# Kernel tuning notes

Measured on AMD Instinct MI355X. Metric: run time of the kernel, lower is better.

Reference implementation:

```python
import jax, jax.numpy as jnp
import numpy as np

EPS = 1e-3  # keras BatchNormalization default epsilon


def _ngf(atoms, bonds, edges, W, b):
    """NeuralGraphHidden: neighbor gather + per-degree dense.
    atoms [B,N,Fa], bonds [B,N,D,Fb], edges [B,N,D] (-1 padded),
    W [D+1, Fa+Fb, width], b [D+1, width] -> [B,N,width]."""
    B, N, Fa = atoms.shape
    D = edges.shape[-1]
    deg = jnp.sum(edges != -1, axis=-1)  # [B,N] atom degrees
    # zero-row padded lookup table so edge index -1 gathers zeros
    apad = jnp.concatenate([jnp.zeros((B, 1, Fa), atoms.dtype), atoms], axis=1)
    neigh = jax.vmap(lambda a, e: a[e])(apad, edges + 1)  # [B,N,D,Fa]
    summed_atom = atoms + neigh.sum(axis=2)  # include_self=True
    summed_bond = bonds.sum(axis=2)
    feats = jnp.concatenate([summed_atom, summed_bond], axis=-1)  # [B,N,Fa+Fb]
    # dense transform for every degree, then select by actual degree
    all_out = jnp.einsum('bnf,dfw->bdnw', feats, W) + b[None, :, None, :]
    mask = (deg[:, None, :] == jnp.arange(D + 1)[None, :, None]).astype(atoms.dtype)
    return jnp.einsum('bdnw,bdn->bnw', all_out, mask)


def _bn(x, g, beta, m, v):
    return g * (x - m) * jax.lax.rsqrt(v + EPS) + beta


def setup_inputs() -> dict:
    key = jax.random.key(0)
    ks = jax.random.split(key, 32)
    B, N, D, Fa, Fb = 1024, 60, 5, 62, 6
    widths = [128, 128, 128]
    KSZ, FILT = 16, 128

    atoms = jax.random.normal(ks[0], (B, N, Fa), jnp.float32)
    bonds = jax.random.uniform(ks[1], (B, N, D, Fb), dtype=jnp.float32)
    edges = jax.random.randint(ks[2], (B, N, D), -1, N).astype(jnp.int32)

    def glorot(k, shape):
        s = jnp.sqrt(2.0 / (shape[-2] + shape[-1])).astype(jnp.float32)
        return jax.random.normal(k, shape, jnp.float32) * s

    inp = dict(atoms=atoms, bonds=bonds, edges=edges)
    fins = [Fa + Fb, widths[0] + Fb, widths[1] + Fb]
    for i in range(3):
        inp['W%d' % (i + 1)] = glorot(ks[3 + i], (D + 1, fins[i], widths[i]))
        inp['b%d' % (i + 1)] = 0.01 * jax.random.normal(ks[6 + i], (D + 1, widths[i]), jnp.float32)
    inp['Wc'] = glorot(ks[9], (KSZ, widths[2], FILT))
    for i, c in enumerate([widths[0], widths[1], widths[2], FILT]):
        inp['bn%d_g' % (i + 1)] = 1.0 + 0.1 * jax.random.normal(ks[10 + i], (c,), jnp.float32)
        inp['bn%d_b' % (i + 1)] = 0.1 * jax.random.normal(ks[14 + i], (c,), jnp.float32)
        inp['bn%d_m' % (i + 1)] = 0.1 * jax.random.normal(ks[18 + i], (c,), jnp.float32)
        inp['bn%d_v' % (i + 1)] = jax.random.uniform(ks[22 + i], (c,), jnp.float32, 0.5, 1.5)
    return inp


def reference(atoms, bonds, edges, W1, b1, W2, b2, W3, b3, Wc,
              bn1_g, bn1_b, bn1_m, bn1_v, bn2_g, bn2_b, bn2_m, bn2_v,
              bn3_g, bn3_b, bn3_m, bn3_v, bn4_g, bn4_b, bn4_m, bn4_v):
    x = jax.nn.relu(_bn(_ngf(atoms, bonds, edges, W1, b1), bn1_g, bn1_b, bn1_m, bn1_v))
    x = jax.nn.relu(_bn(_ngf(x, bonds, edges, W2, b2), bn2_g, bn2_b, bn2_m, bn2_v))
    x = jax.nn.relu(_bn(_ngf(x, bonds, edges, W3, b3), bn3_g, bn3_b, bn3_m, bn3_v))
    # Conv1D over the atom axis, VALID padding, no bias
    x = jax.lax.conv_general_dilated(x, Wc, window_strides=(1,), padding='VALID',
                                     dimension_numbers=('NWC', 'WIO', 'NWC'))
    x = jax.nn.relu(_bn(x, bn4_g, bn4_b, bn4_m, bn4_v))
    # dropout is identity at inference
    return x
```

## Files before the change

kernel.cpp:

```cpp
#include <hip/hip_runtime.h>
#include <hip/hip_bf16.h>

typedef __attribute__((ext_vector_type(8))) short bf16x8;
typedef __attribute__((ext_vector_type(4))) short short4v;
typedef __attribute__((ext_vector_type(4))) float f32x4;
typedef unsigned short u16;
typedef unsigned char u8;

static constexpr size_t OFF_BN   = 0;
static constexpr size_t OFF_SH2  = 4096;
static constexpr size_t OFF_BSUM = 13312;
static constexpr size_t OFF_WT1  = 750592;
static constexpr size_t OFF_WT2  = 898048;
static constexpr size_t OFF_WT3  = 1143808;
static constexpr size_t OFF_WCF  = 1389568;

__device__ __forceinline__ float bf2f(u16 r) {
  union { unsigned u; float f; } cv; cv.u = ((unsigned)r) << 16; return cv.f;
}
__device__ __forceinline__ u16 f2bf(float x) {
  __hip_bfloat16 h = __float2bfloat16(x); return *(u16*)&h;
}
__device__ __forceinline__ int fidx(int n, int c) {
  int u = c >> 3;
  int uu = (u < 16) ? (u ^ (n & 7)) : u;
  return n * 160 + (uu << 3) + (c & 7);
}

__device__ __forceinline__ void emit_wt(u16* dst, const float* W, int FIN, int FIN_A,
                                        int CB, int KSTEPS, int v) {
  int lane = v & 63;
  int ftile = (v >> 6) & 7;
  int ks = (v >> 9) % KSTEPS;
  int d = (v >> 9) / KSTEPS;
  int f = ftile * 16 + (lane & 15);
  int k0 = ks * 32 + (lane >> 4) * 8;
  bf16x8 o;
  #pragma unroll
  for (int i = 0; i < 8; ++i) {
    int k = k0 + i;
    int src = (k < FIN_A) ? k : (k >= CB && k < CB + 6) ? (FIN_A + k - CB) : -1;
    float x = (src >= 0) ? W[((size_t)d * FIN + src) * 128 + f] : 0.f;
    o[i] = (short)f2bf(x);
  }
  *reinterpret_cast<bf16x8*>(&dst[(size_t)v * 8]) = o;
}

__global__ __launch_bounds__(256) void prep(
    const float* __restrict__ bonds, const float* __restrict__ Wc,
    const float* __restrict__ W1, const float* __restrict__ W2, const float* __restrict__ W3,
    const float* g1, const float* be1, const float* m1, const float* v1,
    const float* g2, const float* be2, const float* m2, const float* v2,
    const float* g3, const float* be3, const float* m3, const float* v3,
    const float* g4, const float* be4, const float* m4, const float* v4,
    const float* bb1, const float* bb2, const float* bb3,
    float* __restrict__ scale, float* __restrict__ shift, float* __restrict__ shift2,
    u16* __restrict__ bsum, u16* __restrict__ wt1, u16* __restrict__ wt2,
    u16* __restrict__ wt3, u16* __restrict__ wcf) {
  __shared__ float sb[3840];
  const int b = blockIdx.x, tid = threadIdx.x;
  if (b < 480) {
    const int base = b * 128;
    const float4* src = (const float4*)(bonds + (size_t)base * 30);
    for (int i = tid; i < 960; i += 256) ((float4*)sb)[i] = src[i];
    __syncthreads();
    if (tid < 128) {
      float s[6] = {0.f, 0.f, 0.f, 0.f, 0.f, 0.f};
      #pragma unroll
      for (int d = 0; d < 5; ++d)
        #pragma unroll
        for (int j = 0; j < 6; ++j) s[j] += sb[tid * 30 + d * 6 + j];
      #pragma unroll
      for (int j = 0; j < 6; ++j) bsum[(size_t)(base + tid) * 6 + j] = f2bf(s[j]);
    }
  } else if (b < 608) {
    int v = (b - 480) * 256 + tid;
    int lane = v & 63, ftile = (v >> 6) & 7, ks = v >> 9;
    int f = ftile * 16 + (lane & 15);
    int k0 = ks * 32 + (lane >> 4) * 8;
    int tap = k0 >> 7, ch0 = k0 & 127;
    bf16x8 o;
    #pragma unroll
    for (int i = 0; i < 8; ++i)
      o[i] = (short)f2bf(Wc[((size_t)tap * 128 + ch0 + i) * 128 + f]);
    *reinterpret_cast<bf16x8*>(&wcf[(size_t)v * 8]) = o;
  } else if (b < 644) {
    emit_wt(wt1, W1, 68, 62, 64, 3, (b - 608) * 256 + tid);
  } else if (b < 704) {
    emit_wt(wt2, W2, 134, 128, 128, 5, (b - 644) * 256 + tid);
  } else if (b < 764) {
    emit_wt(wt3, W3, 134, 128, 128, 5, (b - 704) * 256 + tid);
  } else if (b < 766) {
    int idx = (b - 764) * 256 + tid;
    const float* gs[4] = {g1, g2, g3, g4};
    const float* bs[4] = {be1, be2, be3, be4};
    const float* ms[4] = {m1, m2, m3, m4};
    const float* vs[4] = {v1, v2, v3, v4};
    int l = idx >> 7, ch = idx & 127;
    float sc = gs[l][ch] / sqrtf(vs[l][ch] + 1e-3f);
    scale[idx] = sc;
    shift[idx] = bs[l][ch] - ms[l][ch] * sc;
  } else {
    int i = (b - 766) * 256 + tid;
    if (i < 2304) {
      const float* G[3] = {g1, g2, g3};
      const float* Be[3] = {be1, be2, be3};
      const float* M[3] = {m1, m2, m3};
      const float* V[3] = {v1, v2, v3};
      const float* Bl[3] = {bb1, bb2, bb3};
      int ll = i / 768, r = i % 768, f = r & 127;
      float sc = G[ll][f] / sqrtf(V[ll][f] + 1e-3f);
      float sh = Be[ll][f] - M[ll][f] * sc;
      shift2[i] = Bl[ll][r] * sc + sh;
    }
  }
}

template <int MPW, int CB, int KSTEPS, bool TOCONV>
__device__ __forceinline__ void layer(
    u16* __restrict__ feats, u16* __restrict__ xbt,
    const u8* __restrict__ S8, const u8* __restrict__ degs8,
    const int* __restrict__ presentS, const u16* __restrict__ bsum_b,
    const u16* __restrict__ wtf, const float* __restrict__ sc_l,
    const float* __restrict__ sh2_l, int tid, int lane, int wid) {
  const int fr = lane & 15, rg = lane >> 4;

  bf16x8 sf[4][2];
  #pragma unroll
  for (int nt = 0; nt < 4; ++nt) {
    #pragma unroll
    for (int ks = 0; ks < 2; ++ks) {
      int n = nt * 16 + fr, m0 = ks * 32 + rg * 8;
      const unsigned* wp = (const unsigned*)(S8 + n * 64 + m0);
      unsigned lo = wp[0], hi = wp[1];
      bf16x8 v;
      #pragma unroll
      for (int i = 0; i < 4; ++i) v[i] = (short)f2bf((float)((lo >> (i * 8)) & 255u));
      #pragma unroll
      for (int i = 0; i < 4; ++i) v[4 + i] = (short)f2bf((float)((hi >> (i * 8)) & 255u));
      sf[nt][ks] = v;
    }
  }

  f32x4 gacc[MPW][4];
  #pragma unroll
  for (int mt = 0; mt < MPW; ++mt)
    #pragma unroll
    for (int nt = 0; nt < 4; ++nt) gacc[mt][nt] = (f32x4){0.f, 0.f, 0.f, 0.f};
  #pragma unroll
  for (int mt = 0; mt < MPW; ++mt) {
    const int c = (wid * MPW + mt) * 16 + fr;
    #pragma unroll
    for (int ks = 0; ks < 2; ++ks) {
      const int m0 = ks * 32 + rg * 8;
      bf16x8 a = *reinterpret_cast<const bf16x8*>(
          &xbt[c * 64 + (((m0 >> 3) ^ (c & 7)) << 3)]);
      #pragma unroll
      for (int nt = 0; nt < 4; ++nt)
        gacc[mt][nt] = __builtin_amdgcn_mfma_f32_16x16x32_bf16(a, sf[nt][ks],
                                                               gacc[mt][nt], 0, 0, 0);
    }
  }
  #pragma unroll
  for (int mt = 0; mt < MPW; ++mt) {
    const int c0 = (wid * MPW + mt) * 16 + rg * 4;
    const int uu = c0 >> 3;
    #pragma unroll
    for (int nt = 0; nt < 4; ++nt) {
      const int n = nt * 16 + fr;
      if (n < 60) {
        short4v p;
        #pragma unroll
        for (int j = 0; j < 4; ++j) p[j] = (short)f2bf(gacc[mt][nt][j]);
        *reinterpret_cast<short4v*>(
            &feats[n * 160 + ((uu ^ (n & 7)) << 3) + (c0 & 7)]) = p;
      }
    }
  }
  for (int i = tid; i < 360; i += 256) {
    int n = i / 6, c = CB + (i % 6);
    feats[fidx(n, c)] = bsum_b[i];
  }
  __syncthreads();

  const int pres = *presentS;

  if constexpr (!TOCONV) {
    const int f0w = wid * 32;
    unsigned dgw[4];
    #pragma unroll
    for (int m = 0; m < 4; ++m)
      dgw[m] = *(const unsigned*)(degs8 + m * 16 + rg * 4);
    float scf[2] = {sc_l[f0w + fr], sc_l[f0w + 16 + fr]};
    f32x4 racc[4][2];
    #pragma unroll
    for (int m = 0; m < 4; ++m)
      #pragma unroll
      for (int nf = 0; nf < 2; ++nf) racc[m][nf] = (f32x4){0.f, 0.f, 0.f, 0.f};

    for (int d = 0; d < 6; ++d) {
      if (!(pres & (1 << d))) continue;
      const u16* __restrict__ wd = wtf + (size_t)d * (KSTEPS * 4096);
      f32x4 acc[4][2];
      #pragma unroll
      for (int m = 0; m < 4; ++m)
        #pragma unroll
        for (int nf = 0; nf < 2; ++nf) acc[m][nf] = (f32x4){0.f, 0.f, 0.f, 0.f};
      bf16x8 wring[2][2];
      #pragma unroll
      for (int nf = 0; nf < 2; ++nf)
        wring[0][nf] = *reinterpret_cast<const bf16x8*>(
            &wd[((0 * 8 + wid * 2 + nf) * 64 + lane) * 8]);
      #pragma unroll
      for (int nf = 0; nf < 2; ++nf)
        wring[1][nf] = *reinterpret_cast<const bf16x8*>(
            &wd[((1 * 8 + wid * 2 + nf) * 64 + lane) * 8]);
      #pragma unroll
      for (int ks = 0; ks < KSTEPS; ++ks) {
        bf16x8 afr[4];
        const int u = ks * 4 + rg;
        #pragma unroll
        for (int m = 0; m < 4; ++m) {
          const int n = m * 16 + fr;
          const int uu = (u < 16) ? (u ^ (n & 7)) : u;
          afr[m] = *reinterpret_cast<const bf16x8*>(&feats[n * 160 + (uu << 3)]);
        }
        #pragma unroll
        for (int m = 0; m < 4; ++m)
          #pragma unroll
          for (int nf = 0; nf < 2; ++nf)
            acc[m][nf] = __builtin_amdgcn_mfma_f32_16x16x32_bf16(
                afr[m], wring[ks & 1][nf], acc[m][nf], 0, 0, 0);
        if (ks + 2 < KSTEPS) {
          #pragma unroll
          for (int nf = 0; nf < 2; ++nf)
            wring[ks & 1][nf] = *reinterpret_cast<const bf16x8*>(
                &wd[(((ks + 2) * 8 + wid * 2 + nf) * 64 + lane) * 8]);
        }
      }
      #pragma unroll
      for (int nf = 0; nf < 2; ++nf) {
        const float sh = sh2_l[d * 128 + f0w + nf * 16 + fr];
        #pragma unroll
        for (int m = 0; m < 4; ++m) {
          #pragma unroll
          for (int j = 0; j < 4; ++j) {
            float y = fmaxf(acc[m][nf][j] * scf[nf] + sh, 0.f);
            bool sel = (((dgw[m] >> (8 * j)) & 255u) == (unsigned)d);
            racc[m][nf][j] = sel ? y : racc[m][nf][j];
          }
        }
      }
    }
    #pragma unroll
    for (int m = 0; m < 4; ++m) {
      const int n0 = m * 16 + rg * 4;
      if (n0 < 60) {
        #pragma unroll
        for (int nf = 0; nf < 2; ++nf) {
          const int c = f0w + nf * 16 + fr;
          short4v p;
          #pragma unroll
          for (int j = 0; j < 4; ++j) p[j] = (short)f2bf(racc[m][nf][j]);
          *reinterpret_cast<short4v*>(
              &xbt[c * 64 + (((n0 >> 3) ^ (c & 7)) << 3) + (n0 & 7)]) = p;
        }
      }
    }
  } else {
    int dgn[4];
    #pragma unroll
    for (int nt = 0; nt < 4; ++nt) dgn[nt] = degs8[nt * 16 + fr];
    f32x4 scv[2];
    #pragma unroll
    for (int mt = 0; mt < 2; ++mt)
      scv[mt] = *reinterpret_cast<const f32x4*>(&sc_l[(wid * 2 + mt) * 16 + rg * 4]);
    f32x4 racc[2][4];
    #pragma unroll
    for (int mt = 0; mt < 2; ++mt)
      #pragma unroll
      for (int nt = 0; nt < 4; ++nt) racc[mt][nt] = (f32x4){0.f, 0.f, 0.f, 0.f};

    for (int d = 0; d < 6; ++d) {
      if (!(pres & (1 << d))) continue;
      const u16* __restrict__ wd = wtf + (size_t)d * (KSTEPS * 4096);
      f32x4 acc[2][4];
      #pragma unroll
      for (int mt = 0; mt < 2; ++mt)
        #pragma unroll
        for (int nt = 0; nt < 4; ++nt) acc[mt][nt] = (f32x4){0.f, 0.f, 0.f, 0.f};
      bf16x8 wring[2][2];
      #pragma unroll
      for (int mt = 0; mt < 2; ++mt)
        wring[0][mt] = *reinterpret_cast<const bf16x8*>(
            &wd[((0 * 8 + wid * 2 + mt) * 64 + lane) * 8]);
      #pragma unroll
      for (int mt = 0; mt < 2; ++mt)
        wring[1][mt] = *reinterpret_cast<const bf16x8*>(
            &wd[((1 * 8 + wid * 2 + mt) * 64 + lane) * 8]);
      #pragma unroll
      for (int ks = 0; ks < KSTEPS; ++ks) {
        bf16x8 bfr[4];
        const int u = ks * 4 + rg;
        #pragma unroll
        for (int nt = 0; nt < 4; ++nt) {
          const int n = nt * 16 + fr;
          const int uu = (u < 16) ? (u ^ (n & 7)) : u;
          bfr[nt] = *reinterpret_cast<const bf16x8*>(&feats[n * 160 + (uu << 3)]);
        }
        #pragma unroll
        for (int mt = 0; mt < 2; ++mt)
          #pragma unroll
          for (int nt = 0; nt < 4; ++nt)
            acc[mt][nt] = __builtin_amdgcn_mfma_f32_16x16x32_bf16(
                wring[ks & 1][mt], bfr[nt], acc[mt][nt], 0, 0, 0);
        if (ks + 2 < KSTEPS) {
          #pragma unroll
          for (int mt = 0; mt < 2; ++mt)
            wring[ks & 1][mt] = *reinterpret_cast<const bf16x8*>(
                &wd[(((ks + 2) * 8 + wid * 2 + mt) * 64 + lane) * 8]);
        }
      }
      #pragma unroll
      for (int mt = 0; mt < 2; ++mt) {
        f32x4 shv = *reinterpret_cast<const f32x4*>(
            &sh2_l[d * 128 + (wid * 2 + mt) * 16 + rg * 4]);
        #pragma unroll
        for (int nt = 0; nt < 4; ++nt) {
          bool sel = (dgn[nt] == d);
          #pragma unroll
          for (int j = 0; j < 4; ++j) {
            float y = fmaxf(acc[mt][nt][j] * scv[mt][j] + shv[j], 0.f);
            racc[mt][nt][j] = sel ? y : racc[mt][nt][j];
          }
        }
      }
    }
    #pragma unroll
    for (int nt = 0; nt < 4; ++nt) {
      const int n = nt * 16 + fr;
      if (n < 60) {
        #pragma unroll
        for (int mt = 0; mt < 2; ++mt) {
          const int f0 = (wid * 2 + mt) * 16 + rg * 4;
          short4v p;
          #pragma unroll
          for (int j = 0; j < 4; ++j) p[j] = (short)f2bf(racc[mt][nt][j]);
          *reinterpret_cast<short4v*>(
              &xbt[n * 128 + (((f0 >> 3) ^ (n & 7)) << 3) + (f0 & 7)]) = p;
        }
      }
    }
  }
  __syncthreads();
}

__global__ __launch_bounds__(256, 4) void mega(
    const float* __restrict__ atoms, const int* __restrict__ edges_g,
    const u16* __restrict__ bsum, const u16* __restrict__ wt1,
    const u16* __restrict__ wt2, const u16* __restrict__ wt3,
    const u16* __restrict__ wcf, const float* __restrict__ scale,
    const float* __restrict__ shift, const float* __restrict__ shift2,
    float* __restrict__ out) {
  __shared__ __align__(16) char smem[39936];
  u16* feats = (u16*)smem;
  u16* xbt = (u16*)(smem + 19200);
  u8* S8 = (u8*)(smem + 35584);
  signed char* eds = (signed char*)(smem + 39424);
  u8* degs8 = (u8*)(smem + 39728);
  int* presentS = (int*)(smem + 39792);
  float* fscr = (float*)smem;

  const int b = blockIdx.x, tid = threadIdx.x;
  const int lane = tid & 63;
  const int wid = __builtin_amdgcn_readfirstlane(tid >> 6);

  if (tid == 0) *presentS = 0;
  for (int i = tid; i < 300; i += 256) eds[i] = (signed char)edges_g[b * 300 + i];
  {
    const float4* ag4 = (const float4*)(atoms + (size_t)b * 3720);
    float4* fs4 = (float4*)fscr;
    for (int i = tid; i < 930; i += 256) fs4[i] = ag4[i];
    int4 z4 = {0, 0, 0, 0};
    int4* xz = (int4*)(xbt + 64 * 64);
    for (int i = tid; i < 512; i += 256) xz[i] = z4;
    int4* sz = (int4*)S8;
    for (int i = tid; i < 240; i += 256) sz[i] = z4;
  }
  __syncthreads();

  if (tid < 64) {
    int dgv = 7;
    if (tid < 60) {
      dgv = 0;
      #pragma unroll
      for (int d = 0; d < 5; ++d) dgv += (eds[tid * 5 + d] >= 0);
      atomicOr(presentS, 1 << dgv);
      S8[tid * 64 + tid] = (u8)(S8[tid * 64 + tid] + 1);
      #pragma unroll
      for (int d = 0; d < 5; ++d) {
        int e = eds[tid * 5 + d];
        if (e >= 0) S8[tid * 64 + e] = (u8)(S8[tid * 64 + e] + 1);
      }
    }
    degs8[tid] = (u8)dgv;
  }
  for (int id = tid; id < 512; id += 256) {
    int oct = id & 7, c = id >> 3;
    bf16x8 v;
    #pragma unroll
    for (int k = 0; k < 8; ++k) {
      int n = oct * 8 + k;
      float x = (c < 62 && n < 60) ? fscr[n * 62 + c] : 0.f;
      v[k] = (short)f2bf(x);
    }
    *reinterpret_cast<bf16x8*>(&xbt[c * 64 + ((oct ^ (c & 7)) << 3)]) = v;
  }
  __syncthreads();

  for (int i = tid; i < 60 * 52; i += 256) {
    int n = i / 52, q = i % 52;
    int c = (q < 26) ? (70 + q) : (108 + q);
    feats[fidx(n, c)] = 0;
  }

  const u16* bsum_b = bsum + (size_t)b * 360;
  layer<1, 64, 3, false>(feats, xbt, S8, degs8, presentS, bsum_b, wt1,
                         scale + 0, shift2 + 0, tid, lane, wid);
  layer<2, 128, 5, false>(feats, xbt, S8, degs8, presentS, bsum_b, wt2,
                          scale + 128, shift2 + 768, tid, lane, wid);
  layer<2, 128, 5, true>(feats, xbt, S8, degs8, presentS, bsum_b, wt3,
                         scale + 256, shift2 + 1536, tid, lane, wid);

  {
    const int fr = lane & 15, rg = lane >> 4;
    const u16* xconv = xbt;
    f32x4 cacc[3][2];
    #pragma unroll
    for (int rt = 0; rt < 3; ++rt)
      #pragma unroll
      for (int ct = 0; ct < 2; ++ct) cacc[rt][ct] = (f32x4){0.f, 0.f, 0.f, 0.f};

    bf16x8 br[4][2], ar[2][3];
    auto loadB = [&](int ks, int slot) {
      #pragma unroll
      for (int nt = 0; nt < 2; ++nt)
        br[slot][nt] = *reinterpret_cast<const bf16x8*>(
            &wcf[(((size_t)ks * 8 + wid * 2 + nt) * 64 + lane) * 8]);
    };
    auto loadA = [&](int ks, int slot) {
      int rowadd = ks >> 2;
      int unit = ((ks & 3) << 2) + rg;
      #pragma unroll
      for (int rt = 0; rt < 3; ++rt) {
        int arow = rt * 16 + fr + rowadd;
        int uo = unit ^ (arow & 7);
        ar[slot][rt] = *reinterpret_cast<const bf16x8*>(&xconv[arow * 128 + uo * 8]);
      }
    };
    loadB(0, 0); loadB(1, 1); loadB(2, 2); loadA(0, 0);
    #pragma unroll 4
    for (int ks = 0; ks < 64; ++ks) {
      if (ks < 63) loadA(ks + 1, (ks + 1) & 1);
      #pragma unroll
      for (int rt = 0; rt < 3; ++rt)
        #pragma unroll
        for (int ct = 0; ct < 2; ++ct)
          cacc[rt][ct] = __builtin_amdgcn_mfma_f32_16x16x32_bf16(
              ar[ks & 1][rt], br[ks & 3][ct], cacc[rt][ct], 0, 0, 0);
      if (ks < 61) loadB(ks + 3, (ks + 3) & 3);
    }

    #pragma unroll
    for (int ct = 0; ct < 2; ++ct) {
      int f = wid * 32 + ct * 16 + fr;
      float sc = scale[384 + f], sh = shift[384 + f];
      #pragma unroll
      for (int rt = 0; rt < 3; ++rt) {
        #pragma unroll
        for (int j = 0; j < 4; ++j) {
          int t = rt * 16 + rg * 4 + j;
          if (t < 45) {
            float y = fmaxf(cacc[rt][ct][j] * sc + sh, 0.f);
            out[((size_t)b * 45 + t) * 128 + f] = y;
          }
        }
      }
    }
  }
}

extern "C" void kernel_launch(void* const* d_in, const int* in_sizes, int n_in,
                              void* d_out, int out_size, void* d_ws, size_t ws_size,
                              hipStream_t stream) {
  const float* atoms = (const float*)d_in[0];
  const float* bonds = (const float*)d_in[1];
  const int*   edges = (const int*)d_in[2];
  const float* W1 = (const float*)d_in[3]; const float* b1 = (const float*)d_in[4];
  const float* W2 = (const float*)d_in[5]; const float* b2 = (const float*)d_in[6];
  const float* W3 = (const float*)d_in[7]; const float* b3 = (const float*)d_in[8];
  const float* Wc = (const float*)d_in[9];

  char* ws = (char*)d_ws;
  float* scale  = (float*)(ws + OFF_BN);
  float* shift  = scale + 512;
  float* shift2 = (float*)(ws + OFF_SH2);
  u16*   bsum   = (u16*)(ws + OFF_BSUM);
  u16*   wt1    = (u16*)(ws + OFF_WT1);
  u16*   wt2    = (u16*)(ws + OFF_WT2);
  u16*   wt3    = (u16*)(ws + OFF_WT3);
  u16*   wcf    = (u16*)(ws + OFF_WCF);

  prep<<<775, 256, 0, stream>>>(
      bonds, Wc, W1, W2, W3,
      (const float*)d_in[10], (const float*)d_in[11], (const float*)d_in[12], (const float*)d_in[13],
      (const float*)d_in[14], (const float*)d_in[15], (const float*)d_in[16], (const float*)d_in[17],
      (const float*)d_in[18], (const float*)d_in[19], (const float*)d_in[20], (const float*)d_in[21],
      (const float*)d_in[22], (const float*)d_in[23], (const float*)d_in[24], (const float*)d_in[25],
      b1, b2, b3, scale, shift, shift2, bsum, wt1, wt2, wt3, wcf);

  mega<<<1024, 256, 0, stream>>>(atoms, edges, bsum, wt1, wt2, wt3, wcf,
                                 scale, shift, shift2, (float*)d_out);
}
```

Baseline: 202.9 us.

## Process two molecules per block and skip MFMA tiles without matching degree

Each block now handles two molecules with 512 threads, so each wave loads one weight fragment and reuses it across both molecules' atom tiles. A per-degree, per-16-row tile mask is built in shared memory, and MFMAs plus epilogue work are skipped for tiles with no atom of that degree. This cuts weight fetch traffic and redundant matrix work per molecule. In exchange it doubles LDS use per block (about 80KB), which lowers occupancy, and it adds divergent-free but branchy tile checks plus a union of degree-present masks across the two molecules.

```diff
diff --git a/kernel.cpp b/kernel.cpp
--- a/kernel.cpp
+++ b/kernel.cpp
@@ -120,10 +120,15 @@
 __device__ __forceinline__ void layer(
     u16* __restrict__ feats, u16* __restrict__ xbt,
     const u8* __restrict__ S8, const u8* __restrict__ degs8,
-    const int* __restrict__ presentS, const u16* __restrict__ bsum_b,
-    const u16* __restrict__ wtf, const float* __restrict__ sc_l,
-    const float* __restrict__ sh2_l, int tid, int lane, int wid) {
+    const int* __restrict__ presentS, const int* __restrict__ tilemask,
+    const u16* __restrict__ bsum2, const u16* __restrict__ wtf,
+    const float* __restrict__ sc_l, const float* __restrict__ sh2_l,
+    int tid, int lane, int w) {
   const int fr = lane & 15, rg = lane >> 4;
+  const int gmol = w & 1;
+  const u16* __restrict__ xm = xbt + gmol * 8192;
+  u16* __restrict__ fm = feats + gmol * 9600;
+  const u8* __restrict__ Sm = S8 + gmol * 4096;
 
   bf16x8 sf[4][2];
   #pragma unroll
@@ -131,7 +136,7 @@
     #pragma unroll
     for (int ks = 0; ks < 2; ++ks) {
       int n = nt * 16 + fr, m0 = ks * 32 + rg * 8;
-      const unsigned* wp = (const unsigned*)(S8 + n * 64 + m0);
+      const unsigned* wp = (const unsigned*)(Sm + n * 64 + m0);
       unsigned lo = wp[0], hi = wp[1];
       bf16x8 v;
       #pragma unroll
@@ -149,12 +154,12 @@
     for (int nt = 0; nt < 4; ++nt) gacc[mt][nt] = (f32x4){0.f, 0.f, 0.f, 0.f};
   #pragma unroll
   for (int mt = 0; mt < MPW; ++mt) {
-    const int c = (wid * MPW + mt) * 16 + fr;
+    const int c = ((w >> 1) * MPW + mt) * 16 + fr;
     #pragma unroll
     for (int ks = 0; ks < 2; ++ks) {
       const int m0 = ks * 32 + rg * 8;
       bf16x8 a = *reinterpret_cast<const bf16x8*>(
-          &xbt[c * 64 + (((m0 >> 3) ^ (c & 7)) << 3)]);
+          &xm[c * 64 + (((m0 >> 3) ^ (c & 7)) << 3)]);
       #pragma unroll
       for (int nt = 0; nt < 4; ++nt)
         gacc[mt][nt] = __builtin_amdgcn_mfma_f32_16x16x32_bf16(a, sf[nt][ks],
@@ -163,7 +168,7 @@
   }
   #pragma unroll
   for (int mt = 0; mt < MPW; ++mt) {
-    const int c0 = (wid * MPW + mt) * 16 + rg * 4;
+    const int c0 = ((w >> 1) * MPW + mt) * 16 + rg * 4;
     const int uu = c0 >> 3;
     #pragma unroll
     for (int nt = 0; nt < 4; ++nt) {
@@ -173,181 +178,170 @@
         #pragma unroll
         for (int j = 0; j < 4; ++j) p[j] = (short)f2bf(gacc[mt][nt][j]);
         *reinterpret_cast<short4v*>(
-            &feats[n * 160 + ((uu ^ (n & 7)) << 3) + (c0 & 7)]) = p;
-      }
-    }
-  }
-  for (int i = tid; i < 360; i += 256) {
-    int n = i / 6, c = CB + (i % 6);
-    feats[fidx(n, c)] = bsum_b[i];
+            &fm[n * 160 + ((uu ^ (n & 7)) << 3) + (c0 & 7)]) = p;
+      }
+    }
+  }
+  for (int i = tid; i < 720; i += 512) {
+    int m2 = (i >= 360) ? 1 : 0;
+    int j = i - m2 * 360;
+    int n = j / 6, c = CB + (j % 6);
+    feats[m2 * 9600 + fidx(n, c)] = bsum2[m2 * 360 + j];
   }
   __syncthreads();
 
-  const int pres = *presentS;
+  const int presU = __builtin_amdgcn_readfirstlane(presentS[0] | presentS[1]);
+  f32x4 racc[8];
+  #pragma unroll
+  for (int t = 0; t < 8; ++t) racc[t] = (f32x4){0.f, 0.f, 0.f, 0.f};
 
   if constexpr (!TOCONV) {
-    const int f0w = wid * 32;
-    unsigned dgw[4];
-    #pragma unroll
-    for (int m = 0; m < 4; ++m)
-      dgw[m] = *(const unsigned*)(degs8 + m * 16 + rg * 4);
-    float scf[2] = {sc_l[f0w + fr], sc_l[f0w + 16 + fr]};
-    f32x4 racc[4][2];
-    #pragma unroll
-    for (int m = 0; m < 4; ++m)
-      #pragma unroll
-      for (int nf = 0; nf < 2; ++nf) racc[m][nf] = (f32x4){0.f, 0.f, 0.f, 0.f};
+    unsigned dgw[8];
+    #pragma unroll
+    for (int m2 = 0; m2 < 2; ++m2)
+      #pragma unroll
+      for (int nt = 0; nt < 4; ++nt)
+        dgw[m2 * 4 + nt] = *(const unsigned*)(degs8 + m2 * 64 + nt * 16 + rg * 4);
+    const float scf = sc_l[w * 16 + fr];
 
     for (int d = 0; d < 6; ++d) {
-      if (!(pres & (1 << d))) continue;
+      if (!(presU & (1 << d))) continue;
+      const int tm0 = __builtin_amdgcn_readfirstlane(tilemask[d]);
+      const int tm1 = __builtin_amdgcn_readfirstlane(tilemask[6 + d]);
       const u16* __restrict__ wd = wtf + (size_t)d * (KSTEPS * 4096);
-      f32x4 acc[4][2];
-      #pragma unroll
-      for (int m = 0; m < 4; ++m)
-        #pragma unroll
-        for (int nf = 0; nf < 2; ++nf) acc[m][nf] = (f32x4){0.f, 0.f, 0.f, 0.f};
-      bf16x8 wring[2][2];
-      #pragma unroll
-      for (int nf = 0; nf < 2; ++nf)
-        wring[0][nf] = *reinterpret_cast<const bf16x8*>(
-            &wd[((0 * 8 + wid * 2 + nf) * 64 + lane) * 8]);
-      #pragma unroll
-      for (int nf = 0; nf < 2; ++nf)
-        wring[1][nf] = *reinterpret_cast<const bf16x8*>(
-            &wd[((1 * 8 + wid * 2 + nf) * 64 + lane) * 8]);
+      f32x4 acc[8];
+      #pragma unroll
+      for (int t = 0; t < 8; ++t) acc[t] = (f32x4){0.f, 0.f, 0.f, 0.f};
+      bf16x8 wring[2];
+      wring[0] = *reinterpret_cast<const bf16x8*>(&wd[((0 * 8 + w) * 64 + lane) * 8]);
+      wring[1] = *reinterpret_cast<const bf16x8*>(&wd[((1 * 8 + w) * 64 + lane) * 8]);
       #pragma unroll
       for (int ks = 0; ks < KSTEPS; ++ks) {
-        bf16x8 afr[4];
         const int u = ks * 4 + rg;
         #pragma unroll
-        for (int m = 0; m < 4; ++m) {
-          const int n = m * 16 + fr;
-          const int uu = (u < 16) ? (u ^ (n & 7)) : u;
-          afr[m] = *reinterpret_cast<const bf16x8*>(&feats[n * 160 + (uu << 3)]);
-        }
-        #pragma unroll
-        for (int m = 0; m < 4; ++m)
+        for (int m2 = 0; m2 < 2; ++m2) {
+          const int tmv = m2 ? tm1 : tm0;
           #pragma unroll
-          for (int nf = 0; nf < 2; ++nf)
-            acc[m][nf] = __builtin_amdgcn_mfma_f32_16x16x32_bf16(
-                afr[m], wring[ks & 1][nf], acc[m][nf], 0, 0, 0);
-        if (ks + 2 < KSTEPS) {
-          #pragma unroll
-          for (int nf = 0; nf < 2; ++nf)
-            wring[ks & 1][nf] = *reinterpret_cast<const bf16x8*>(
-                &wd[(((ks + 2) * 8 + wid * 2 + nf) * 64 + lane) * 8]);
-        }
-      }
-      #pragma unroll
-      for (int nf = 0; nf < 2; ++nf) {
-        const float sh = sh2_l[d * 128 + f0w + nf * 16 + fr];
-        #pragma unroll
-        for (int m = 0; m < 4; ++m) {
-          #pragma unroll
-          for (int j = 0; j < 4; ++j) {
-            float y = fmaxf(acc[m][nf][j] * scf[nf] + sh, 0.f);
-            bool sel = (((dgw[m] >> (8 * j)) & 255u) == (unsigned)d);
-            racc[m][nf][j] = sel ? y : racc[m][nf][j];
+          for (int nt = 0; nt < 4; ++nt) {
+            if (tmv & (1 << nt)) {
+              const int n = nt * 16 + fr;
+              const int uu = (u < 16) ? (u ^ (n & 7)) : u;
+              bf16x8 afr = *reinterpret_cast<const bf16x8*>(
+                  &feats[m2 * 9600 + n * 160 + (uu << 3)]);
+              acc[m2 * 4 + nt] = __builtin_amdgcn_mfma_f32_16x16x32_bf16(
+                  afr, wring[ks & 1], acc[m2 * 4 + nt], 0, 0, 0);
+            }
           }
         }
-      }
-    }
-    #pragma unroll
-    for (int m = 0; m < 4; ++m) {
-      const int n0 = m * 16 + rg * 4;
-      if (n0 < 60) {
-        #pragma unroll
-        for (int nf = 0; nf < 2; ++nf) {
-          const int c = f0w + nf * 16 + fr;
+        if (ks + 2 < KSTEPS)
+          wring[ks & 1] = *reinterpret_cast<const bf16x8*>(
+              &wd[(((ks + 2) * 8 + w) * 64 + lane) * 8]);
+      }
+      const float sh = sh2_l[d * 128 + w * 16 + fr];
+      #pragma unroll
+      for (int m2 = 0; m2 < 2; ++m2) {
+        const int tmv = m2 ? tm1 : tm0;
+        #pragma unroll
+        for (int nt = 0; nt < 4; ++nt) {
+          if (tmv & (1 << nt)) {
+            const int tt = m2 * 4 + nt;
+            #pragma unroll
+            for (int j = 0; j < 4; ++j) {
+              float y = fmaxf(acc[tt][j] * scf + sh, 0.f);
+              bool sel = (((dgw[tt] >> (8 * j)) & 255u) == (unsigned)d);
+              racc[tt][j] = sel ? y : racc[tt][j];
+            }
+          }
+        }
+      }
+    }
+    #pragma unroll
+    for (int m2 = 0; m2 < 2; ++m2) {
+      #pragma unroll
+      for (int nt = 0; nt < 4; ++nt) {
+        const int n0 = nt * 16 + rg * 4;
+        if (n0 < 60) {
+          const int c = w * 16 + fr;
           short4v p;
           #pragma unroll
-          for (int j = 0; j < 4; ++j) p[j] = (short)f2bf(racc[m][nf][j]);
+          for (int j = 0; j < 4; ++j) p[j] = (short)f2bf(racc[m2 * 4 + nt][j]);
           *reinterpret_cast<short4v*>(
-              &xbt[c * 64 + (((n0 >> 3) ^ (c & 7)) << 3) + (n0 & 7)]) = p;
+              &xbt[m2 * 8192 + c * 64 + (((n0 >> 3) ^ (c & 7)) << 3) + (n0 & 7)]) = p;
         }
       }
     }
   } else {
-    int dgn[4];
-    #pragma unroll
-    for (int nt = 0; nt < 4; ++nt) dgn[nt] = degs8[nt * 16 + fr];
-    f32x4 scv[2];
-    #pragma unroll
-    for (int mt = 0; mt < 2; ++mt)
-      scv[mt] = *reinterpret_cast<const f32x4*>(&sc_l[(wid * 2 + mt) * 16 + rg * 4]);
-    f32x4 racc[2][4];
-    #pragma unroll
-    for (int mt = 0; mt < 2; ++mt)
-      #pragma unroll
-      for (int nt = 0; nt < 4; ++nt) racc[mt][nt] = (f32x4){0.f, 0.f, 0.f, 0.f};
+    int dgn[8];
+    #pragma unroll
+    for (int m2 = 0; m2 < 2; ++m2)
+      #pragma unroll
+      for (int nt = 0; nt < 4; ++nt)
+        dgn[m2 * 4 + nt] = degs8[m2 * 64 + nt * 16 + fr];
+    f32x4 scv = *reinterpret_cast<const f32x4*>(&sc_l[w * 16 + rg * 4]);
 
     for (int d = 0; d < 6; ++d) {
-      if (!(pres & (1 << d))) continue;
+      if (!(presU & (1 << d))) continue;
+      const int tm0 = __builtin_amdgcn_readfirstlane(tilemask[d]);
+      const int tm1 = __builtin_amdgcn_readfirstlane(tilemask[6 + d]);
       const u16* __restrict__ wd = wtf + (size_t)d * (KSTEPS * 4096);
-      f32x4 acc[2][4];
-      #pragma unroll
-      for (int mt = 0; mt < 2; ++mt)
-        #pragma unroll
-        for (int nt = 0; nt < 4; ++nt) acc[mt][nt] = (f32x4){0.f, 0.f, 0.f, 0.f};
-      bf16x8 wring[2][2];
-      #pragma unroll
-      for (int mt = 0; mt < 2; ++mt)
-        wring[0][mt] = *reinterpret_cast<const bf16x8*>(
-            &wd[((0 * 8 + wid * 2 + mt) * 64 + lane) * 8]);
-      #pragma unroll
-      for (int mt = 0; mt < 2; ++mt)
-        wring[1][mt] = *reinterpret_cast<const bf16x8*>(
-            &wd[((1 * 8 + wid * 2 + mt) * 64 + lane) * 8]);
+      f32x4 acc[8];
+      #pragma unroll
+      for (int t = 0; t < 8; ++t) acc[t] = (f32x4){0.f, 0.f, 0.f, 0.f};
+      bf16x8 wring[2];
+      wring[0] = *reinterpret_cast<const bf16x8*>(&wd[((0 * 8 + w) * 64 + lane) * 8]);
+      wring[1] = *reinterpret_cast<const bf16x8*>(&wd[((1 * 8 + w) * 64 + lane) * 8]);
       #pragma unroll
       for (int ks = 0; ks < KSTEPS; ++ks) {
-        bf16x8 bfr[4];
         const int u = ks * 4 + rg;
         #pragma unroll
+        for (int m2 = 0; m2 < 2; ++m2) {
+          const int tmv = m2 ? tm1 : tm0;
+          #pragma unroll
+          for (int nt = 0; nt < 4; ++nt) {
+            if (tmv & (1 << nt)) {
+              const int n = nt * 16 + fr;
+              const int uu = (u < 16) ? (u ^ (n & 7)) : u;
+              bf16x8 bfr = *reinterpret_cast<const bf16x8*>(
+                  &feats[m2 * 9600 + n * 160 + (uu << 3)]);
+              acc[m2 * 4 + nt] = __builtin_amdgcn_mfma_f32_16x16x32_bf16(
+                  wring[ks & 1], bfr, acc[m2 * 4 + nt], 0, 0, 0);
+            }
+          }
+        }
+        if (ks + 2 < KSTEPS)
+          wring[ks & 1] = *reinterpret_cast<const bf16x8*>(
+              &wd[(((ks + 2) * 8 + w) * 64 + lane) * 8]);
+      }
+      f32x4 shv = *reinterpret_cast<const f32x4*>(&sh2_l[d * 128 + w * 16 + rg * 4]);
+      #pragma unroll
+      for (int m2 = 0; m2 < 2; ++m2) {
+        const int tmv = m2 ? tm1 : tm0;
+        #pragma unroll
         for (int nt = 0; nt < 4; ++nt) {
-          const int n = nt * 16 + fr;
-          const int uu = (u < 16) ? (u ^ (n & 7)) : u;
-          bfr[nt] = *reinterpret_cast<const bf16x8*>(&feats[n * 160 + (uu << 3)]);
-        }
-        #pragma unroll
-        for (int mt = 0; mt < 2; ++mt)
-          #pragma unroll
-          for (int nt = 0; nt < 4; ++nt)
-            acc[mt][nt] = __builtin_amdgcn_mfma_f32_16x16x32_bf16(
-                wring[ks & 1][mt], bfr[nt], acc[mt][nt], 0, 0, 0);
-        if (ks + 2 < KSTEPS) {
-          #pragma unroll
-          for (int mt = 0; mt < 2; ++mt)
-            wring[ks & 1][mt] = *reinterpret_cast<const bf16x8*>(
-                &wd[(((ks + 2) * 8 + wid * 2 + mt) * 64 + lane) * 8]);
-        }
-      }
-      #pragma unroll
-      for (int mt = 0; mt < 2; ++mt) {
-        f32x4 shv = *reinterpret_cast<const f32x4*>(
-            &sh2_l[d * 128 + (wid * 2 + mt) * 16 + rg * 4]);
-        #pragma unroll
-        for (int nt = 0; nt < 4; ++nt) {
-          bool sel = (dgn[nt] == d);
-          #pragma unroll
-          for (int j = 0; j < 4; ++j) {
-            float y = fmaxf(acc[mt][nt][j] * scv[mt][j] + shv[j], 0.f);
-            racc[mt][nt][j] = sel ? y : racc[mt][nt][j];
+          if (tmv & (1 << nt)) {
+            const int tt = m2 * 4 + nt;
+            bool sel = (dgn[tt] == d);
+            #pragma unroll
+            for (int j = 0; j < 4; ++j) {
+              float y = fmaxf(acc[tt][j] * scv[j] + shv[j], 0.f);
+              racc[tt][j] = sel ? y : racc[tt][j];
+            }
           }
         }
       }
     }
     #pragma unroll
-    for (int nt = 0; nt < 4; ++nt) {
-      const int n = nt * 16 + fr;
-      if (n < 60) {
-        #pragma unroll
-        for (int mt = 0; mt < 2; ++mt) {
-          const int f0 = (wid * 2 + mt) * 16 + rg * 4;
+    for (int m2 = 0; m2 < 2; ++m2) {
+      #pragma unroll
+      for (int nt = 0; nt < 4; ++nt) {
+        const int n = nt * 16 + fr;
+        if (n < 60) {
+          const int f0 = w * 16 + rg * 4;
           short4v p;
           #pragma unroll
-          for (int j = 0; j < 4; ++j) p[j] = (short)f2bf(racc[mt][nt][j]);
+          for (int j = 0; j < 4; ++j) p[j] = (short)f2bf(racc[m2 * 4 + nt][j]);
           *reinterpret_cast<short4v*>(
-              &xbt[n * 128 + (((f0 >> 3) ^ (n & 7)) << 3) + (f0 & 7)]) = p;
+              &xbt[m2 * 8192 + n * 128 + (((f0 >> 3) ^ (n & 7)) << 3) + (f0 & 7)]) = p;
         }
       }
     }
@@ -355,107 +349,131 @@
   __syncthreads();
 }
 
-__global__ __launch_bounds__(256, 4) void mega(
+__global__ __launch_bounds__(512, 4) void mega(
     const float* __restrict__ atoms, const int* __restrict__ edges_g,
     const u16* __restrict__ bsum, const u16* __restrict__ wt1,
     const u16* __restrict__ wt2, const u16* __restrict__ wt3,
     const u16* __restrict__ wcf, const float* __restrict__ scale,
     const float* __restrict__ shift, const float* __restrict__ shift2,
     float* __restrict__ out) {
-  __shared__ __align__(16) char smem[39936];
+  __shared__ __align__(16) char smem[80160];
   u16* feats = (u16*)smem;
-  u16* xbt = (u16*)(smem + 19200);
-  u8* S8 = (u8*)(smem + 35584);
-  signed char* eds = (signed char*)(smem + 39424);
-  u8* degs8 = (u8*)(smem + 39728);
-  int* presentS = (int*)(smem + 39792);
-  float* fscr = (float*)smem;
-
-  const int b = blockIdx.x, tid = threadIdx.x;
+  u16* xbt = (u16*)(smem + 38400);
+  u8* S8 = (u8*)(smem + 71168);
+  signed char* eds = (signed char*)(smem + 79360);
+  u8* degs8 = (u8*)(smem + 79960);
+  int* presentS = (int*)(smem + 80088);
+  int* tilemask = (int*)(smem + 80096);
+
+  const int b0 = blockIdx.x * 2, tid = threadIdx.x;
   const int lane = tid & 63;
-  const int wid = __builtin_amdgcn_readfirstlane(tid >> 6);
-
-  if (tid == 0) *presentS = 0;
-  for (int i = tid; i < 300; i += 256) eds[i] = (signed char)edges_g[b * 300 + i];
+  const int w = __builtin_amdgcn_readfirstlane(tid >> 6);
+
+  if (tid < 2) presentS[tid] = 0;
+  if (tid >= 2 && tid < 14) tilemask[tid - 2] = 0;
+  for (int i = tid; i < 600; i += 512) eds[i] = (signed char)edges_g[b0 * 300 + i];
   {
-    const float4* ag4 = (const float4*)(atoms + (size_t)b * 3720);
-    float4* fs4 = (float4*)fscr;
-    for (int i = tid; i < 930; i += 256) fs4[i] = ag4[i];
-    int4 z4 = {0, 0, 0, 0};
-    int4* xz = (int4*)(xbt + 64 * 64);
-    for (int i = tid; i < 512; i += 256) xz[i] = z4;
+    int4 z = {0, 0, 0, 0};
     int4* sz = (int4*)S8;
-    for (int i = tid; i < 240; i += 256) sz[i] = z4;
+    for (int i = tid; i < 512; i += 512) sz[i] = z;
+    int4* x0 = (int4*)(xbt + 4096);
+    int4* x1 = (int4*)(xbt + 8192 + 4096);
+    for (int i = tid; i < 512; i += 512) { x0[i] = z; x1[i] = z; }
+    const float4* ag = (const float4*)(atoms + (size_t)b0 * 3720);
+    float4* fs0 = (float4*)feats;
+    float4* fs1 = (float4*)(feats + 9600);
+    for (int i = tid; i < 1860; i += 512) {
+      float4 v = ag[i];
+      if (i < 930) fs0[i] = v; else fs1[i - 930] = v;
+    }
   }
   __syncthreads();
 
-  if (tid < 64) {
-    int dgv = 7;
-    if (tid < 60) {
-      dgv = 0;
-      #pragma unroll
-      for (int d = 0; d < 5; ++d) dgv += (eds[tid * 5 + d] >= 0);
-      atomicOr(presentS, 1 << dgv);
-      S8[tid * 64 + tid] = (u8)(S8[tid * 64 + tid] + 1);
-      #pragma unroll
-      for (int d = 0; d < 5; ++d) {
-        int e = eds[tid * 5 + d];
-        if (e >= 0) S8[tid * 64 + e] = (u8)(S8[tid * 64 + e] + 1);
-      }
-    }
-    degs8[tid] = (u8)dgv;
-  }
-  for (int id = tid; id < 512; id += 256) {
-    int oct = id & 7, c = id >> 3;
+  for (int id = tid; id < 1024; id += 512) {
+    int mol = id >> 9, r = id & 511;
+    int oct = r & 7, c = r >> 3;
+    const float* fs = (const float*)(feats + mol * 9600);
     bf16x8 v;
     #pragma unroll
     for (int k = 0; k < 8; ++k) {
       int n = oct * 8 + k;
-      float x = (c < 62 && n < 60) ? fscr[n * 62 + c] : 0.f;
+      float x = (c < 62 && n < 60) ? fs[n * 62 + c] : 0.f;
       v[k] = (short)f2bf(x);
     }
-    *reinterpret_cast<bf16x8*>(&xbt[c * 64 + ((oct ^ (c & 7)) << 3)]) = v;
+    *reinterpret_cast<bf16x8*>(&xbt[mol * 8192 + c * 64 + ((oct ^ (c & 7)) << 3)]) = v;
+  }
+  if (tid < 128) {
+    int mol = tid >> 6, n = tid & 63;
+    int dgv = 7;
+    if (n < 60) {
+      dgv = 0;
+      const signed char* e = eds + mol * 300 + n * 5;
+      #pragma unroll
+      for (int d = 0; d < 5; ++d) dgv += (e[d] >= 0);
+      atomicOr(&presentS[mol], 1 << dgv);
+      u8* Sm = S8 + mol * 4096;
+      Sm[n * 64 + n] = (u8)(Sm[n * 64 + n] + 1);
+      #pragma unroll
+      for (int d = 0; d < 5; ++d) {
+        int ev = e[d];
+        if (ev >= 0) Sm[n * 64 + ev] = (u8)(Sm[n * 64 + ev] + 1);
+      }
+    }
+    degs8[tid] = (u8)dgv;
   }
   __syncthreads();
 
-  for (int i = tid; i < 60 * 52; i += 256) {
-    int n = i / 52, q = i % 52;
-    int c = (q < 26) ? (70 + q) : (108 + q);
-    feats[fidx(n, c)] = 0;
-  }
-
-  const u16* bsum_b = bsum + (size_t)b * 360;
-  layer<1, 64, 3, false>(feats, xbt, S8, degs8, presentS, bsum_b, wt1,
-                         scale + 0, shift2 + 0, tid, lane, wid);
-  layer<2, 128, 5, false>(feats, xbt, S8, degs8, presentS, bsum_b, wt2,
-                          scale + 128, shift2 + 768, tid, lane, wid);
-  layer<2, 128, 5, true>(feats, xbt, S8, degs8, presentS, bsum_b, wt3,
-                         scale + 256, shift2 + 1536, tid, lane, wid);
+  {
+    int4 z = {0, 0, 0, 0};
+    int4* fz = (int4*)feats;
+    for (int i = tid; i < 2400; i += 512) fz[i] = z;
+  }
+  if (tid < 48) {
+    int m2 = tid / 24, rem = tid % 24, d = rem >> 2, nt = rem & 3;
+    bool any = false;
+    #pragma unroll
+    for (int r = 0; r < 15; ++r) {
+      int n = nt * 16 + r;
+      if (n < 60 && degs8[m2 * 64 + n] == (u8)d) any = true;
+    }
+    { int n = nt * 16 + 15; if (n < 60 && degs8[m2 * 64 + n] == (u8)d) any = true; }
+    if (any) atomicOr(&tilemask[m2 * 6 + d], 1 << nt);
+  }
+  __syncthreads();
+
+  const u16* bsum2 = bsum + (size_t)b0 * 360;
+  layer<1, 64, 3, false>(feats, xbt, S8, degs8, presentS, tilemask, bsum2, wt1,
+                         scale + 0, shift2 + 0, tid, lane, w);
+  layer<2, 128, 5, false>(feats, xbt, S8, degs8, presentS, tilemask, bsum2, wt2,
+                          scale + 128, shift2 + 768, tid, lane, w);
+  layer<2, 128, 5, true>(feats, xbt, S8, degs8, presentS, tilemask, bsum2, wt3,
+                         scale + 256, shift2 + 1536, tid, lane, w);
 
   {
     const int fr = lane & 15, rg = lane >> 4;
-    const u16* xconv = xbt;
-    f32x4 cacc[3][2];
-    #pragma unroll
-    for (int rt = 0; rt < 3; ++rt)
-      #pragma unroll
-      for (int ct = 0; ct < 2; ++ct) cacc[rt][ct] = (f32x4){0.f, 0.f, 0.f, 0.f};
-
-    bf16x8 br[4][2], ar[2][3];
+    f32x4 cacc[2][3];
+    #pragma unroll
+    for (int m2 = 0; m2 < 2; ++m2)
+      #pragma unroll
+      for (int rt = 0; rt < 3; ++rt) cacc[m2][rt] = (f32x4){0.f, 0.f, 0.f, 0.f};
+
+    bf16x8 br[4], ar[2][2][3];
     auto loadB = [&](int ks, int slot) {
-      #pragma unroll
-      for (int nt = 0; nt < 2; ++nt)
-        br[slot][nt] = *reinterpret_cast<const bf16x8*>(
-            &wcf[(((size_t)ks * 8 + wid * 2 + nt) * 64 + lane) * 8]);
+      br[slot] = *reinterpret_cast<const bf16x8*>(
+          &wcf[(((size_t)ks * 8 + w) * 64 + lane) * 8]);
     };
     auto loadA = [&](int ks, int slot) {
       int rowadd = ks >> 2;
       int unit = ((ks & 3) << 2) + rg;
       #pragma unroll
-      for (int rt = 0; rt < 3; ++rt) {
-        int arow = rt * 16 + fr + rowadd;
-        int uo = unit ^ (arow & 7);
-        ar[slot][rt] = *reinterpret_cast<const bf16x8*>(&xconv[arow * 128 + uo * 8]);
+      for (int m2 = 0; m2 < 2; ++m2) {
+        #pragma unroll
+        for (int rt = 0; rt < 3; ++rt) {
+          int arow = rt * 16 + fr + rowadd;
+          int uo = unit ^ (arow & 7);
+          ar[slot][m2][rt] = *reinterpret_cast<const bf16x8*>(
+              &xbt[m2 * 8192 + arow * 128 + uo * 8]);
+        }
       }
     };
     loadB(0, 0); loadB(1, 1); loadB(2, 2); loadA(0, 0);
@@ -463,26 +481,26 @@
     for (int ks = 0; ks < 64; ++ks) {
       if (ks < 63) loadA(ks + 1, (ks + 1) & 1);
       #pragma unroll
-      for (int rt = 0; rt < 3; ++rt)
-        #pragma unroll
-        for (int ct = 0; ct < 2; ++ct)
-          cacc[rt][ct] = __builtin_amdgcn_mfma_f32_16x16x32_bf16(
-              ar[ks & 1][rt], br[ks & 3][ct], cacc[rt][ct], 0, 0, 0);
+      for (int m2 = 0; m2 < 2; ++m2)
+        #pragma unroll
+        for (int rt = 0; rt < 3; ++rt)
+          cacc[m2][rt] = __builtin_amdgcn_mfma_f32_16x16x32_bf16(
+              ar[ks & 1][m2][rt], br[ks & 3], cacc[m2][rt], 0, 0, 0);
       if (ks < 61) loadB(ks + 3, (ks + 3) & 3);
     }
 
-    #pragma unroll
-    for (int ct = 0; ct < 2; ++ct) {
-      int f = wid * 32 + ct * 16 + fr;
-      float sc = scale[384 + f], sh = shift[384 + f];
+    const int f = w * 16 + fr;
+    const float sc = scale[384 + f], sh = shift[384 + f];
+    #pragma unroll
+    for (int m2 = 0; m2 < 2; ++m2) {
       #pragma unroll
       for (int rt = 0; rt < 3; ++rt) {
         #pragma unroll
         for (int j = 0; j < 4; ++j) {
           int t = rt * 16 + rg * 4 + j;
           if (t < 45) {
-            float y = fmaxf(cacc[rt][ct][j] * sc + sh, 0.f);
-            out[((size_t)b * 45 + t) * 128 + f] = y;
+            float y = fmaxf(cacc[m2][rt][j] * sc + sh, 0.f);
+            out[((size_t)(b0 + m2) * 45 + t) * 128 + f] = y;
           }
         }
       }
@@ -519,6 +537,6 @@
       (const float*)d_in[22], (const float*)d_in[23], (const float*)d_in[24], (const float*)d_in[25],
       b1, b2, b3, scale, shift, shift2, bsum, wt1, wt2, wt3, wcf);
 
-  mega<<<1024, 256, 0, stream>>>(atoms, edges, bsum, wt1, wt2, wt3, wcf,
-                                 scale, shift, shift2, (float*)d_out);
-}
+  mega<<<512, 512, 0, stream>>>(atoms, edges, bsum, wt1, wt2, wt3, wcf,
+                                scale, shift, shift2, (float*)d_out);
+}
```

New measurement: 200.8 us. About the same (-1.0%).
